# Optimization experiments

Hardware: AMD Instinct MI355X
Metric: run time of the kernel (lower is better)

The kernel has to match this reference:

```python
import jax, jax.numpy as jnp
import numpy as np

N_NODES = 100000
N_EDGES = 1600000
IN_C, HID_C, OUT_C = 64, 128, 64


def _sage_conv(x, src, dst, Wl, bl, Wr, n_nodes):
    # PyG SAGEConv (mean aggr): out = lin_l(mean_{j in N(i)} x_j) + lin_r(x_i)
    msg = x[src]  # [E, C] gather
    agg = jax.ops.segment_sum(msg, dst, num_segments=n_nodes)
    deg = jax.ops.segment_sum(jnp.ones((src.shape[0],), x.dtype), dst, num_segments=n_nodes)
    agg = agg / jnp.maximum(deg, 1.0)[:, None]
    return agg @ Wl + bl + x @ Wr


def setup_inputs() -> dict:
    key = jax.random.key(0)
    ks = jax.random.split(key, 16)
    x = jax.random.normal(ks[0], (N_NODES, IN_C), dtype=jnp.float32)
    edge_index = jax.random.randint(ks[1], (2, N_EDGES), 0, N_NODES, dtype=jnp.int64)
    s = 0.05
    return {
        "x": x,
        "edge_index": edge_index,
        # conv1: SAGEConv(IN_C, HID_C)
        "Wl1": jax.random.normal(ks[2], (IN_C, HID_C), jnp.float32) * s,
        "bl1": jnp.zeros((HID_C,), jnp.float32),
        "Wr1": jax.random.normal(ks[3], (IN_C, HID_C), jnp.float32) * s,
        # conv2: SAGEConv(HID_C, OUT_C)
        "Wl2": jax.random.normal(ks[4], (HID_C, OUT_C), jnp.float32) * s,
        "bl2": jnp.zeros((OUT_C,), jnp.float32),
        "Wr2": jax.random.normal(ks[5], (HID_C, OUT_C), jnp.float32) * s,
        # classifier MLP: OUT_C -> HID_C -> HID_C//2 -> 1
        "Wc1": jax.random.normal(ks[6], (OUT_C, HID_C), jnp.float32) * s,
        "bc1": jnp.zeros((HID_C,), jnp.float32),
        "Wc2": jax.random.normal(ks[7], (HID_C, HID_C // 2), jnp.float32) * s,
        "bc2": jnp.zeros((HID_C // 2,), jnp.float32),
        "Wc3": jax.random.normal(ks[8], (HID_C // 2, 1), jnp.float32) * s,
        "bc3": jnp.zeros((1,), jnp.float32),
    }


def reference(x, edge_index, Wl1, bl1, Wr1, Wl2, bl2, Wr2, Wc1, bc1, Wc2, bc2, Wc3, bc3):
    src, dst = edge_index[0], edge_index[1]
    n = x.shape[0]
    h = _sage_conv(x, src, dst, Wl1, bl1, Wr1, n)
    h = jax.nn.relu(h)  # dropout is identity in eval mode
    embeddings = _sage_conv(h, src, dst, Wl2, bl2, Wr2, n)
    # classifier head
    c = jax.nn.relu(embeddings @ Wc1 + bc1)
    c = jax.nn.relu(c @ Wc2 + bc2)
    fraud_probs = jax.nn.sigmoid(c @ Wc3 + bc3)
    return embeddings, fraud_probs
```

## Files before the change

### kernel.cpp

```cpp
#include <hip/hip_runtime.h>
#include <math.h>

#define N_NODES 100000
#define ZERO_NODE 100000
#define N_EDGES 1600000
#define NBKT    391
#define BCAP    5120
#define EPB     4096
#define NBLKA   391
#define PADBKT  768
#define BUCKET_CAP (N_EDGES + NBKT * PADBKT + BCAP)

using short8  = __attribute__((ext_vector_type(8))) short;
using float4v = __attribute__((ext_vector_type(4))) float;

__device__ inline unsigned short f2bf(float f) {
    unsigned int u = __float_as_uint(f);
    u += 0x7fffu + ((u >> 16) & 1u);
    return (unsigned short)(u >> 16);
}
__device__ inline float bflo(unsigned int v) { return __uint_as_float(v << 16); }
__device__ inline float bfhi(unsigned int v) { return __uint_as_float(v & 0xffff0000u); }

__global__ void prep_all(const float* __restrict__ x, unsigned short* __restrict__ xb,
                         const float* __restrict__ Wl1, const float* __restrict__ Wr1,
                         const float* __restrict__ Wl2, const float* __restrict__ Wr2,
                         const float* __restrict__ Wc1, const float* __restrict__ Wc2,
                         unsigned short* __restrict__ w1, unsigned short* __restrict__ w2,
                         unsigned short* __restrict__ wcls1, unsigned short* __restrict__ wcls2,
                         unsigned short* __restrict__ t2b) {
    int bid = blockIdx.x;
    int t = threadIdx.x;
    if (bid < 6250) {
        int i = bid * 256 + t;
        float4 v = *(const float4*)(x + (long)i * 4);
        uint2 o;
        o.x = (unsigned)f2bf(v.x) | ((unsigned)f2bf(v.y) << 16);
        o.y = (unsigned)f2bf(v.z) | ((unsigned)f2bf(v.w) << 16);
        *(uint2*)(xb + (long)i * 4) = o;
    } else if (bid < 6442) {
        int i = (bid - 6250) * 256 + t;
        if (i < 16384) {
            int n = i >> 7, k = i & 127;
            float v = (k < 64) ? Wl1[k * 128 + n] : Wr1[(k - 64) * 128 + n];
            w1[i] = f2bf(v);
        } else if (i < 32768) {
            int j = i - 16384; int n = j >> 7, k = j & 127;
            float v = (n < 64) ? Wl2[k * 64 + n] : Wr2[k * 64 + (n - 64)];
            w2[j] = f2bf(v);
        } else if (i < 40960) {
            int j = i - 32768; int n = j >> 6, k = j & 63;
            wcls1[j] = f2bf(Wc1[k * 128 + n]);
        } else {
            int j = i - 40960; int n = j >> 7, k = j & 127;
            wcls2[j] = f2bf(Wc2[k * 64 + n]);
        }
    } else {
        if (t < 32)       ((unsigned*)(xb  + (long)ZERO_NODE * 64))[t]      = 0u;
        else if (t < 64)  ((unsigned*)(t2b + (long)ZERO_NODE * 64))[t - 32] = 0u;
    }
}

__global__ __launch_bounds__(256) void binA(const int* __restrict__ esrc,
                                            const int* __restrict__ edst,
                                            int* __restrict__ bcnt,
                                            unsigned* __restrict__ stage) {
    __shared__ int hist[NBKT];
    __shared__ int rbase[NBKT];
    int t = threadIdx.x;
    for (int i = t; i < NBKT; i += 256) hist[i] = 0;
    __syncthreads();
    int e0 = blockIdx.x * EPB;
    int e1 = e0 + EPB; if (e1 > N_EDGES) e1 = N_EDGES;
    unsigned pk[16];
    int bn[16];
#pragma unroll
    for (int j = 0; j < 16; j++) {
        int e = e0 + j * 256 + t;
        bn[j] = -1;
        if (e < N_EDGES && e < e1) {
            int d = edst[e];
            int s = esrc[e];
            int b = d >> 8;
            pk[j] = (unsigned)s | ((unsigned)(d & 255) << 24);
            bn[j] = b;
            atomicAdd(&hist[b], 1);
        }
    }
    __syncthreads();
    for (int i = t; i < NBKT; i += 256) {
        int c = hist[i];
        rbase[i] = c ? atomicAdd(&bcnt[i], c) : 0;
        hist[i] = 0;
    }
    __syncthreads();
#pragma unroll
    for (int j = 0; j < 16; j++) {
        if (bn[j] >= 0) {
            int b = bn[j];
            int slot = rbase[b] + atomicAdd(&hist[b], 1);
            if (slot < BCAP)
                stage[(long)b * BCAP + slot] = pk[j];
        }
    }
}

__global__ __launch_bounds__(256) void binB(const int* __restrict__ bcnt,
                                            const unsigned* __restrict__ stage,
                                            int* __restrict__ offp, int* __restrict__ deg,
                                            int* __restrict__ bucket) {
    __shared__ int sg[512];
    __shared__ int hist[256];
    __shared__ int scn[256];
    __shared__ int lbase[256];
    int b = blockIdx.x, t = threadIdx.x;
    sg[t]       = (t < NBKT) ? bcnt[t] : 0;
    sg[t + 256] = (t + 256 < NBKT) ? bcnt[t + 256] : 0;
    hist[t] = 0;
    __syncthreads();
    for (int st = 1; st < 512; st <<= 1) {
        int a0 = (t >= st) ? sg[t - st] : 0;
        int a1 = (t + 256 >= st) ? sg[t + 256 - st] : 0;
        __syncthreads();
        sg[t] += a0; sg[t + 256] += a1;
        __syncthreads();
    }
    int cntraw = bcnt[b];
    int base = (sg[b] - cntraw) + b * PADBKT;
    int cnt = cntraw > BCAP ? BCAP : cntraw;
    const unsigned* sp = stage + (long)b * BCAP;
    unsigned pk[20];
    int nv = 0;
#pragma unroll
    for (int j = 0; j < 20; j++) {
        int i = j * 256 + t;
        if (i < cnt) {
            pk[j] = sp[i];
            atomicAdd(&hist[pk[j] >> 24], 1);
            nv = j + 1;
        }
    }
    __syncthreads();
    int v = hist[t];
    int p4 = (v + 3) & ~3;
    scn[t] = p4;
    __syncthreads();
    for (int st = 1; st < 256; st <<= 1) {
        int a = (t >= st) ? scn[t - st] : 0;
        __syncthreads();
        scn[t] += a;
        __syncthreads();
    }
    lbase[t] = scn[t] - p4;
    int node = b * 256 + t;
    if (node < N_NODES) {
        offp[node] = base + lbase[t];
        deg[node]  = v;
    }
    hist[t] = 0;
    __syncthreads();
#pragma unroll
    for (int j = 0; j < 20; j++) {
        if (j < nv) {
            unsigned p = pk[j];
            int ln = p >> 24;
            int slot = atomicAdd(&hist[ln], 1);
            bucket[base + lbase[ln] + slot] = (int)(p & 0xFFFFFFu);
        }
    }
    int ps = base + lbase[t] + v;
    int pe = base + lbase[t] + p4;
    for (int j = ps; j < pe; j++) bucket[j] = ZERO_NODE;
}

__global__ __launch_bounds__(256, 8) void gather_b(
        const unsigned short* __restrict__ y, const int* __restrict__ offp,
        const int* __restrict__ deg, const int* __restrict__ bucket,
        unsigned short* __restrict__ outb) {
    int t = threadIdx.x;
    int wv = t >> 6, lane = t & 63;
    int nh = lane >> 5;
    int g  = (lane >> 3) & 3;
    int c8 = lane & 7;
    int node = blockIdx.x * 8 + wv * 2 + nh;
    int e0 = offp[node];
    int dg = deg[node];
    int len = (dg + 3) & ~3;
    int maxlen = max(len, __shfl_xor(len, 32));
    const char* yb = (const char*)y;
    float a[8] = {0.f, 0.f, 0.f, 0.f, 0.f, 0.f, 0.f, 0.f};
    for (int base = 0; base < maxlen; base += 16) {
        uint4 v[4];
#pragma unroll
        for (int h = 0; h < 4; h++) {
            int rel = base + h * 4 + g;
            int s = bucket[e0 + rel];
            s = (rel < len) ? s : ZERO_NODE;
            unsigned off32 = ((unsigned)s << 7) + ((unsigned)c8 << 4);
            v[h] = *(const uint4*)(yb + off32);
        }
#pragma unroll
        for (int h = 0; h < 4; h++) {
            a[0] += bflo(v[h].x); a[1] += bfhi(v[h].x);
            a[2] += bflo(v[h].y); a[3] += bfhi(v[h].y);
            a[4] += bflo(v[h].z); a[5] += bfhi(v[h].z);
            a[6] += bflo(v[h].w); a[7] += bfhi(v[h].w);
        }
    }
#pragma unroll
    for (int j = 0; j < 8; j++) {
        a[j] += __shfl_xor(a[j], 8);
        a[j] += __shfl_xor(a[j], 16);
    }
    if (g == 0) {
        float sc = 1.f / fmaxf((float)dg, 1.f);
        uint4 o;
        o.x = (unsigned)f2bf(a[0]*sc) | ((unsigned)f2bf(a[1]*sc) << 16);
        o.y = (unsigned)f2bf(a[2]*sc) | ((unsigned)f2bf(a[3]*sc) << 16);
        o.z = (unsigned)f2bf(a[4]*sc) | ((unsigned)f2bf(a[5]*sc) << 16);
        o.w = (unsigned)f2bf(a[6]*sc) | ((unsigned)f2bf(a[7]*sc) << 16);
        *(uint4*)(outb + (long)node * 64 + c8 * 8) = o;
    }
}

__global__ __launch_bounds__(256, 8) void gather_badd(
        const unsigned short* __restrict__ y, const int* __restrict__ offp,
        const int* __restrict__ deg, const int* __restrict__ bucket,
        const unsigned short* __restrict__ ub, float* __restrict__ out) {
    int t = threadIdx.x;
    int wv = t >> 6, lane = t & 63;
    int nh = lane >> 5;
    int g  = (lane >> 3) & 3;
    int c8 = lane & 7;
    int node = blockIdx.x * 8 + wv * 2 + nh;
    int e0 = offp[node];
    int dg = deg[node];
    int len = (dg + 3) & ~3;
    int maxlen = max(len, __shfl_xor(len, 32));
    const char* yb = (const char*)y;
    float a[8] = {0.f, 0.f, 0.f, 0.f, 0.f, 0.f, 0.f, 0.f};
    for (int base = 0; base < maxlen; base += 16) {
        uint4 v[4];
#pragma unroll
        for (int h = 0; h < 4; h++) {
            int rel = base + h * 4 + g;
            int s = bucket[e0 + rel];
            s = (rel < len) ? s : ZERO_NODE;
            unsigned off32 = ((unsigned)s << 7) + ((unsigned)c8 << 4);
            v[h] = *(const uint4*)(yb + off32);
        }
#pragma unroll
        for (int h = 0; h < 4; h++) {
            a[0] += bflo(v[h].x); a[1] += bfhi(v[h].x);
            a[2] += bflo(v[h].y); a[3] += bfhi(v[h].y);
            a[4] += bflo(v[h].z); a[5] += bfhi(v[h].z);
            a[6] += bflo(v[h].w); a[7] += bfhi(v[h].w);
        }
    }
#pragma unroll
    for (int j = 0; j < 8; j++) {
        a[j] += __shfl_xor(a[j], 8);
        a[j] += __shfl_xor(a[j], 16);
    }
    if (g == 0) {
        float sc = 1.f / fmaxf((float)dg, 1.f);
        uint2 uv = *(const uint2*)(ub + (long)node * 64 + c8 * 8);
        float4 r0 = { a[0]*sc + bflo(uv.x), a[1]*sc + bfhi(uv.x),
                      a[2]*sc + bflo(uv.y), a[3]*sc + bfhi(uv.y) };
        uint2 uw = *(const uint2*)(ub + (long)node * 64 + c8 * 8 + 4);
        float4 r1 = { a[4]*sc + bflo(uw.x), a[5]*sc + bfhi(uw.x),
                      a[6]*sc + bflo(uw.y), a[7]*sc + bfhi(uw.y) };
        float4* op = (float4*)(out + (long)node * 64 + c8 * 8);
        op[0] = r0; op[1] = r1;
    }
}

__global__ __launch_bounds__(256, 4) void fused_conv(
        const unsigned short* __restrict__ xb, const unsigned short* __restrict__ aggb,
        const unsigned short* __restrict__ w1, const float* __restrict__ bl1,
        const unsigned short* __restrict__ w2, const float* __restrict__ bl2,
        unsigned short* __restrict__ t2b, unsigned short* __restrict__ ub) {
    __shared__ __align__(16) unsigned short smemA[64 * 136];
    __shared__ __align__(16) unsigned short smemH[64 * 136];
    unsigned short* sA = smemA;
    unsigned short* sH = smemH;
    unsigned short* stu = smemA;
    unsigned short* st2 = smemH;

    int t = threadIdx.x;
    int lane = t & 63;
    int wv = t >> 6;
    int q = lane >> 4, ln = lane & 15;

    long base = (long)blockIdx.x * 4096;
    long maxe = (long)N_NODES * 64 - 8;
#pragma unroll
    for (int it = 0; it < 2; it++) {
        int i = it * 256 + t;
        int m = i >> 3, k8 = (i & 7) * 8;
        long g = base + (long)m * 64 + k8;
        if (g > maxe) g = maxe;
        *(uint4*)(sA + m * 136 + k8)      = *(const uint4*)(aggb + g);
        *(uint4*)(sA + m * 136 + 64 + k8) = *(const uint4*)(xb + g);
    }
    __syncthreads();

    int n0 = wv * 32;
    float4v acc[2][4];
    {
        float b0 = bl1[n0 + ln], b1 = bl1[n0 + 16 + ln];
#pragma unroll
        for (int mi = 0; mi < 4; mi++) {
            acc[0][mi] = (float4v){b0, b0, b0, b0};
            acc[1][mi] = (float4v){b1, b1, b1, b1};
        }
    }
#pragma unroll
    for (int ks = 0; ks < 4; ks++) {
        int k0 = ks * 32 + q * 8;
        short8 bf0 = *(const short8*)(w1 + (long)(n0 + ln) * 128 + k0);
        short8 bf1 = *(const short8*)(w1 + (long)(n0 + 16 + ln) * 128 + k0);
#pragma unroll
        for (int mi = 0; mi < 4; mi++) {
            short8 af = *(const short8*)(sA + (mi * 16 + ln) * 136 + k0);
            acc[0][mi] = __builtin_amdgcn_mfma_f32_16x16x32_bf16(af, bf0, acc[0][mi], 0, 0, 0);
            acc[1][mi] = __builtin_amdgcn_mfma_f32_16x16x32_bf16(af, bf1, acc[1][mi], 0, 0, 0);
        }
    }
#pragma unroll
    for (int j = 0; j < 2; j++)
#pragma unroll
        for (int mi = 0; mi < 4; mi++) {
            int n = n0 + j * 16 + ln;
#pragma unroll
            for (int r = 0; r < 4; r++) {
                int m = mi * 16 + q * 4 + r;
                sH[m * 136 + n] = f2bf(fmaxf(acc[j][mi][r], 0.f));
            }
        }
    __syncthreads();

    float4v acc2[2][4];
    {
        float c0 = (n0 >= 64) ? bl2[n0 - 64 + ln] : 0.f;
        float c1 = (n0 >= 64) ? bl2[n0 - 48 + ln] : 0.f;
#pragma unroll
        for (int mi = 0; mi < 4; mi++) {
            acc2[0][mi] = (float4v){c0, c0, c0, c0};
            acc2[1][mi] = (float4v){c1, c1, c1, c1};
        }
    }
#pragma unroll
    for (int ks = 0; ks < 4; ks++) {
        int k0 = ks * 32 + q * 8;
        short8 bf0 = *(const short8*)(w2 + (long)(n0 + ln) * 128 + k0);
        short8 bf1 = *(const short8*)(w2 + (long)(n0 + 16 + ln) * 128 + k0);
#pragma unroll
        for (int mi = 0; mi < 4; mi++) {
            short8 af = *(const short8*)(sH + (mi * 16 + ln) * 136 + k0);
            acc2[0][mi] = __builtin_amdgcn_mfma_f32_16x16x32_bf16(af, bf0, acc2[0][mi], 0, 0, 0);
            acc2[1][mi] = __builtin_amdgcn_mfma_f32_16x16x32_bf16(af, bf1, acc2[1][mi], 0, 0, 0);
        }
    }
    __syncthreads();

#pragma unroll
    for (int j = 0; j < 2; j++)
#pragma unroll
        for (int mi = 0; mi < 4; mi++) {
            int n = n0 + j * 16 + ln;
#pragma unroll
            for (int r = 0; r < 4; r++) {
                int m = mi * 16 + q * 4 + r;
                if (wv < 2) st2[m * 72 + n] = f2bf(acc2[j][mi][r]);
                else        stu[m * 72 + (n - 64)] = f2bf(acc2[j][mi][r]);
            }
        }
    __syncthreads();

    long lim2 = (long)N_NODES * 32;
    unsigned* t2u = (unsigned*)t2b;
    unsigned* uu  = (unsigned*)ub;
    long ubase = base >> 1;
#pragma unroll
    for (int it = 0; it < 8; it++) {
        int i = it * 256 + t;
        long gq = ubase + i;
        if (gq < lim2) {
            int m = (i * 2) >> 6, n = (i * 2) & 63;
            t2u[gq] = (unsigned)st2[m * 72 + n] | ((unsigned)st2[m * 72 + n + 1] << 16);
            uu[gq]  = (unsigned)stu[m * 72 + n] | ((unsigned)stu[m * 72 + n + 1] << 16);
        }
    }
}

__global__ __launch_bounds__(256, 4) void fused_cls(
        const float* __restrict__ emb,
        const unsigned short* __restrict__ wcls1, const float* __restrict__ bc1,
        const unsigned short* __restrict__ wcls2, const float* __restrict__ bc2,
        const float* __restrict__ wc3, const float* __restrict__ bc3,
        float* __restrict__ probs) {
    __shared__ __align__(16) unsigned short smem[64 * 136];
    __shared__ float psum[4][64];
    unsigned short* sE = smem;
    unsigned short* sC = smem;

    int t = threadIdx.x;
    int wv = t >> 6;
    int lane = t & 63;
    int q = lane >> 4, ln = lane & 15;

    long base = (long)blockIdx.x * 4096;
    long maxe = (long)N_NODES * 64 - 4;
#pragma unroll
    for (int it = 0; it < 4; it++) {
        int i = it * 256 + t;
        int m = i >> 4, k4 = (i & 15) * 4;
        long g = base + (long)m * 64 + k4;
        if (g > maxe) g = maxe;
        float4 v = *(const float4*)(emb + g);
        uint2 o;
        o.x = (unsigned)f2bf(v.x) | ((unsigned)f2bf(v.y) << 16);
        o.y = (unsigned)f2bf(v.z) | ((unsigned)f2bf(v.w) << 16);
        *(uint2*)(sE + m * 72 + k4) = o;
    }
    __syncthreads();

    int n0 = wv * 32;
    float4v acc[2][4];
    {
        float b0 = bc1[n0 + ln], b1 = bc1[n0 + 16 + ln];
#pragma unroll
        for (int mi = 0; mi < 4; mi++) {
            acc[0][mi] = (float4v){b0, b0, b0, b0};
            acc[1][mi] = (float4v){b1, b1, b1, b1};
        }
    }
#pragma unroll
    for (int ks = 0; ks < 2; ks++) {
        int k0 = ks * 32 + q * 8;
        short8 bf0 = *(const short8*)(wcls1 + (long)(n0 + ln) * 64 + k0);
        short8 bf1 = *(const short8*)(wcls1 + (long)(n0 + 16 + ln) * 64 + k0);
#pragma unroll
        for (int mi = 0; mi < 4; mi++) {
            short8 af = *(const short8*)(sE + (mi * 16 + ln) * 72 + k0);
            acc[0][mi] = __builtin_amdgcn_mfma_f32_16x16x32_bf16(af, bf0, acc[0][mi], 0, 0, 0);
            acc[1][mi] = __builtin_amdgcn_mfma_f32_16x16x32_bf16(af, bf1, acc[1][mi], 0, 0, 0);
        }
    }
    __syncthreads();
#pragma unroll
    for (int j = 0; j < 2; j++)
#pragma unroll
        for (int mi = 0; mi < 4; mi++) {
            int n = n0 + j * 16 + ln;
#pragma unroll
            for (int r = 0; r < 4; r++) {
                int m = mi * 16 + q * 4 + r;
                sC[m * 136 + n] = f2bf(fmaxf(acc[j][mi][r], 0.f));
            }
        }
    __syncthreads();

    int n0c = wv * 16;
    float4v acc3[4];
    {
        float b = bc2[n0c + ln];
#pragma unroll
        for (int mi = 0; mi < 4; mi++) acc3[mi] = (float4v){b, b, b, b};
    }
#pragma unroll
    for (int ks = 0; ks < 4; ks++) {
        int k0 = ks * 32 + q * 8;
        short8 bf0 = *(const short8*)(wcls2 + (long)(n0c + ln) * 128 + k0);
#pragma unroll
        for (int mi = 0; mi < 4; mi++) {
            short8 af = *(const short8*)(sC + (mi * 16 + ln) * 136 + k0);
            acc3[mi] = __builtin_amdgcn_mfma_f32_16x16x32_bf16(af, bf0, acc3[mi], 0, 0, 0);
        }
    }
    float w3 = wc3[n0c + ln];
#pragma unroll
    for (int mi = 0; mi < 4; mi++)
#pragma unroll
        for (int r = 0; r < 4; r++) {
            float v = fmaxf(acc3[mi][r], 0.f) * w3;
            v += __shfl_xor(v, 1);
            v += __shfl_xor(v, 2);
            v += __shfl_xor(v, 4);
            v += __shfl_xor(v, 8);
            if (ln == 0) psum[wv][mi * 16 + q * 4 + r] = v;
        }
    __syncthreads();
    if (t < 64) {
        int node = blockIdx.x * 64 + t;
        if (node < N_NODES) {
            float tot = psum[0][t] + psum[1][t] + psum[2][t] + psum[3][t] + bc3[0];
            probs[node] = 1.f / (1.f + expf(-tot));
        }
    }
}

extern "C" void kernel_launch(void* const* d_in, const int* in_sizes, int n_in,
                              void* d_out, int out_size, void* d_ws, size_t ws_size,
                              hipStream_t stream) {
    const float* x   = (const float*)d_in[0];
    const int*   ei  = (const int*)d_in[1];
    const float* Wl1 = (const float*)d_in[2];
    const float* bl1 = (const float*)d_in[3];
    const float* Wr1 = (const float*)d_in[4];
    const float* Wl2 = (const float*)d_in[5];
    const float* bl2 = (const float*)d_in[6];
    const float* Wr2 = (const float*)d_in[7];
    const float* Wc1 = (const float*)d_in[8];
    const float* bc1 = (const float*)d_in[9];
    const float* Wc2 = (const float*)d_in[10];
    const float* bc2 = (const float*)d_in[11];
    const float* Wc3 = (const float*)d_in[12];
    const float* bc3 = (const float*)d_in[13];

    float* out = (float*)d_out;

    int* iw     = (int*)d_ws;
    int* bcnt   = iw;
    int* offp   = iw + 1024;
    int* deg    = iw + 1024 + 100352;
    int* bucket = iw + 1024 + 2 * 100352;
    unsigned* stage = (unsigned*)(bucket + BUCKET_CAP);
    size_t ioff = ((size_t)(1024 + 2 * 100352 + BUCKET_CAP) + (size_t)NBKT * BCAP) * 4;
    ioff = (ioff + 127) & ~(size_t)127;

    char* wsb = (char*)d_ws;
    unsigned short* xb    = (unsigned short*)(wsb + ioff);
    unsigned short* agg1b = xb + 6400064L;
    unsigned short* t2b   = agg1b + 6400000L;
    unsigned short* ub    = t2b + 6400064L;
    unsigned short* w1    = ub + 6400000L;
    unsigned short* w2    = w1 + 16384;
    unsigned short* wcls1 = w2 + 16384;
    unsigned short* wcls2 = wcls1 + 8192;

    float* emb   = out;
    float* probs = out + 6400000L;

    const int* esrc = ei;
    const int* edst = ei + N_EDGES;

    hipMemsetAsync(bcnt, 0, 1024 * sizeof(int), stream);

    prep_all<<<6443, 256, 0, stream>>>(x, xb, Wl1, Wr1, Wl2, Wr2, Wc1, Wc2,
                                       w1, w2, wcls1, wcls2, t2b);

    binA<<<NBLKA, 256, 0, stream>>>(esrc, edst, bcnt, stage);
    binB<<<NBKT, 256, 0, stream>>>(bcnt, stage, offp, deg, bucket);

    gather_b<<<12500, 256, 0, stream>>>(xb, offp, deg, bucket, agg1b);
    fused_conv<<<1563, 256, 0, stream>>>(xb, agg1b, w1, bl1, w2, bl2, t2b, ub);
    gather_badd<<<12500, 256, 0, stream>>>(t2b, offp, deg, bucket, ub, emb);
    fused_cls<<<1563, 256, 0, stream>>>(emb, wcls1, bc1, wcls2, bc2, Wc3, bc3, probs);
}
```

Before: 245.7 us.

## Gather neighbor features in fp8 instead of bf16 for both SAGE aggregations

Adds fp8 (e4m3) copies of x and of the layer-2 projected features, and makes both gather kernels read 64-byte fp8 rows instead of 128-byte bf16 rows. Each lane now covers 16 channels and each wave processes 8 edges per step, so node segments are padded to multiples of 8 and the bucket padding grows to match. The intent is to halve the random-gather memory traffic that dominates the aggregation kernels. The cost is extra quantization error from fp8 on the aggregated messages, which could exceed the accuracy tolerance.

```diff
diff --git a/kernel.cpp b/kernel.cpp
--- a/kernel.cpp
+++ b/kernel.cpp
@@ -8,11 +8,12 @@
 #define BCAP    5120
 #define EPB     4096
 #define NBLKA   391
-#define PADBKT  768
-#define BUCKET_CAP (N_EDGES + NBKT * PADBKT + BCAP)
+#define PADBKT  1792
+#define BUCKET_CAP (N_EDGES + NBKT * PADBKT + 2 * BCAP)
 
 using short8  = __attribute__((ext_vector_type(8))) short;
 using float4v = __attribute__((ext_vector_type(4))) float;
+using floatx2 = __attribute__((ext_vector_type(2))) float;
 
 __device__ inline unsigned short f2bf(float f) {
     unsigned int u = __float_as_uint(f);
@@ -21,14 +22,22 @@
 }
 __device__ inline float bflo(unsigned int v) { return __uint_as_float(v << 16); }
 __device__ inline float bfhi(unsigned int v) { return __uint_as_float(v & 0xffff0000u); }
+__device__ inline unsigned char f2fp8(float f) {
+    return (unsigned char)(__builtin_amdgcn_cvt_pk_fp8_f32(f, f, 0, false) & 0xff);
+}
+__device__ inline unsigned pk4fp8(float a, float b, float c, float d) {
+    unsigned p = __builtin_amdgcn_cvt_pk_fp8_f32(a, b, 0, false);
+    return __builtin_amdgcn_cvt_pk_fp8_f32(c, d, p, true);
+}
 
 __global__ void prep_all(const float* __restrict__ x, unsigned short* __restrict__ xb,
+                         unsigned* __restrict__ xq,
                          const float* __restrict__ Wl1, const float* __restrict__ Wr1,
                          const float* __restrict__ Wl2, const float* __restrict__ Wr2,
                          const float* __restrict__ Wc1, const float* __restrict__ Wc2,
                          unsigned short* __restrict__ w1, unsigned short* __restrict__ w2,
                          unsigned short* __restrict__ wcls1, unsigned short* __restrict__ wcls2,
-                         unsigned short* __restrict__ t2b) {
+                         unsigned* __restrict__ t2q) {
     int bid = blockIdx.x;
     int t = threadIdx.x;
     if (bid < 6250) {
@@ -38,6 +47,7 @@
         o.x = (unsigned)f2bf(v.x) | ((unsigned)f2bf(v.y) << 16);
         o.y = (unsigned)f2bf(v.z) | ((unsigned)f2bf(v.w) << 16);
         *(uint2*)(xb + (long)i * 4) = o;
+        xq[i] = pk4fp8(v.x, v.y, v.z, v.w);
     } else if (bid < 6442) {
         int i = (bid - 6250) * 256 + t;
         if (i < 16384) {
@@ -56,8 +66,9 @@
             wcls2[j] = f2bf(Wc2[k * 64 + n]);
         }
     } else {
-        if (t < 32)       ((unsigned*)(xb  + (long)ZERO_NODE * 64))[t]      = 0u;
-        else if (t < 64)  ((unsigned*)(t2b + (long)ZERO_NODE * 64))[t - 32] = 0u;
+        if (t < 32)       ((unsigned*)(xb + (long)ZERO_NODE * 64))[t] = 0u;
+        else if (t < 48)  xq[(long)ZERO_NODE * 16 + (t - 32)] = 0u;
+        else if (t < 64)  t2q[(long)ZERO_NODE * 16 + (t - 48)] = 0u;
     }
 }
 
@@ -142,8 +153,8 @@
     }
     __syncthreads();
     int v = hist[t];
-    int p4 = (v + 3) & ~3;
-    scn[t] = p4;
+    int p8 = (v + 7) & ~7;
+    scn[t] = p8;
     __syncthreads();
     for (int st = 1; st < 256; st <<= 1) {
         int a = (t >= st) ? scn[t - st] : 0;
@@ -151,7 +162,7 @@
         scn[t] += a;
         __syncthreads();
     }
-    lbase[t] = scn[t] - p4;
+    lbase[t] = scn[t] - p8;
     int node = b * 256 + t;
     if (node < N_NODES) {
         offp[node] = base + lbase[t];
@@ -169,109 +180,136 @@
         }
     }
     int ps = base + lbase[t] + v;
-    int pe = base + lbase[t] + p4;
+    int pe = base + lbase[t] + p8;
     for (int j = ps; j < pe; j++) bucket[j] = ZERO_NODE;
 }
 
 __global__ __launch_bounds__(256, 8) void gather_b(
-        const unsigned short* __restrict__ y, const int* __restrict__ offp,
+        const unsigned char* __restrict__ yq, const int* __restrict__ offp,
         const int* __restrict__ deg, const int* __restrict__ bucket,
         unsigned short* __restrict__ outb) {
     int t = threadIdx.x;
     int wv = t >> 6, lane = t & 63;
     int nh = lane >> 5;
-    int g  = (lane >> 3) & 3;
-    int c8 = lane & 7;
+    int g  = (lane >> 2) & 7;
+    int c16 = lane & 3;
     int node = blockIdx.x * 8 + wv * 2 + nh;
     int e0 = offp[node];
     int dg = deg[node];
-    int len = (dg + 3) & ~3;
-    int maxlen = max(len, __shfl_xor(len, 32));
-    const char* yb = (const char*)y;
-    float a[8] = {0.f, 0.f, 0.f, 0.f, 0.f, 0.f, 0.f, 0.f};
-    for (int base = 0; base < maxlen; base += 16) {
+    int len = (dg + 7) & ~7;
+    int other = __shfl_xor(len, 32);
+    int maxlen = len > other ? len : other;
+    float a[16];
+#pragma unroll
+    for (int j = 0; j < 16; j++) a[j] = 0.f;
+    for (int base = 0; base < maxlen; base += 32) {
         uint4 v[4];
 #pragma unroll
         for (int h = 0; h < 4; h++) {
-            int rel = base + h * 4 + g;
+            int rel = base + h * 8 + g;
             int s = bucket[e0 + rel];
             s = (rel < len) ? s : ZERO_NODE;
-            unsigned off32 = ((unsigned)s << 7) + ((unsigned)c8 << 4);
-            v[h] = *(const uint4*)(yb + off32);
+            unsigned off = ((unsigned)s << 6) + ((unsigned)c16 << 4);
+            v[h] = *(const uint4*)(yq + off);
         }
 #pragma unroll
         for (int h = 0; h < 4; h++) {
-            a[0] += bflo(v[h].x); a[1] += bfhi(v[h].x);
-            a[2] += bflo(v[h].y); a[3] += bfhi(v[h].y);
-            a[4] += bflo(v[h].z); a[5] += bfhi(v[h].z);
-            a[6] += bflo(v[h].w); a[7] += bfhi(v[h].w);
-        }
-    }
-#pragma unroll
-    for (int j = 0; j < 8; j++) {
+            floatx2 d;
+            d = __builtin_amdgcn_cvt_pk_f32_fp8(v[h].x, false); a[0] += d.x;  a[1] += d.y;
+            d = __builtin_amdgcn_cvt_pk_f32_fp8(v[h].x, true);  a[2] += d.x;  a[3] += d.y;
+            d = __builtin_amdgcn_cvt_pk_f32_fp8(v[h].y, false); a[4] += d.x;  a[5] += d.y;
+            d = __builtin_amdgcn_cvt_pk_f32_fp8(v[h].y, true);  a[6] += d.x;  a[7] += d.y;
+            d = __builtin_amdgcn_cvt_pk_f32_fp8(v[h].z, false); a[8] += d.x;  a[9] += d.y;
+            d = __builtin_amdgcn_cvt_pk_f32_fp8(v[h].z, true);  a[10] += d.x; a[11] += d.y;
+            d = __builtin_amdgcn_cvt_pk_f32_fp8(v[h].w, false); a[12] += d.x; a[13] += d.y;
+            d = __builtin_amdgcn_cvt_pk_f32_fp8(v[h].w, true);  a[14] += d.x; a[15] += d.y;
+        }
+    }
+#pragma unroll
+    for (int j = 0; j < 16; j++) {
+        a[j] += __shfl_xor(a[j], 4);
         a[j] += __shfl_xor(a[j], 8);
         a[j] += __shfl_xor(a[j], 16);
     }
     if (g == 0) {
         float sc = 1.f / fmaxf((float)dg, 1.f);
-        uint4 o;
-        o.x = (unsigned)f2bf(a[0]*sc) | ((unsigned)f2bf(a[1]*sc) << 16);
-        o.y = (unsigned)f2bf(a[2]*sc) | ((unsigned)f2bf(a[3]*sc) << 16);
-        o.z = (unsigned)f2bf(a[4]*sc) | ((unsigned)f2bf(a[5]*sc) << 16);
-        o.w = (unsigned)f2bf(a[6]*sc) | ((unsigned)f2bf(a[7]*sc) << 16);
-        *(uint4*)(outb + (long)node * 64 + c8 * 8) = o;
+        uint4 o0, o1;
+        o0.x = (unsigned)f2bf(a[0]*sc)  | ((unsigned)f2bf(a[1]*sc) << 16);
+        o0.y = (unsigned)f2bf(a[2]*sc)  | ((unsigned)f2bf(a[3]*sc) << 16);
+        o0.z = (unsigned)f2bf(a[4]*sc)  | ((unsigned)f2bf(a[5]*sc) << 16);
+        o0.w = (unsigned)f2bf(a[6]*sc)  | ((unsigned)f2bf(a[7]*sc) << 16);
+        o1.x = (unsigned)f2bf(a[8]*sc)  | ((unsigned)f2bf(a[9]*sc) << 16);
+        o1.y = (unsigned)f2bf(a[10]*sc) | ((unsigned)f2bf(a[11]*sc) << 16);
+        o1.z = (unsigned)f2bf(a[12]*sc) | ((unsigned)f2bf(a[13]*sc) << 16);
+        o1.w = (unsigned)f2bf(a[14]*sc) | ((unsigned)f2bf(a[15]*sc) << 16);
+        unsigned short* op = outb + (long)node * 64 + c16 * 16;
+        *(uint4*)op = o0;
+        *(uint4*)(op + 8) = o1;
     }
 }
 
 __global__ __launch_bounds__(256, 8) void gather_badd(
-        const unsigned short* __restrict__ y, const int* __restrict__ offp,
+        const unsigned char* __restrict__ yq, const int* __restrict__ offp,
         const int* __restrict__ deg, const int* __restrict__ bucket,
         const unsigned short* __restrict__ ub, float* __restrict__ out) {
     int t = threadIdx.x;
     int wv = t >> 6, lane = t & 63;
     int nh = lane >> 5;
-    int g  = (lane >> 3) & 3;
-    int c8 = lane & 7;
+    int g  = (lane >> 2) & 7;
+    int c16 = lane & 3;
     int node = blockIdx.x * 8 + wv * 2 + nh;
     int e0 = offp[node];
     int dg = deg[node];
-    int len = (dg + 3) & ~3;
-    int maxlen = max(len, __shfl_xor(len, 32));
-    const char* yb = (const char*)y;
-    float a[8] = {0.f, 0.f, 0.f, 0.f, 0.f, 0.f, 0.f, 0.f};
-    for (int base = 0; base < maxlen; base += 16) {
+    int len = (dg + 7) & ~7;
+    int other = __shfl_xor(len, 32);
+    int maxlen = len > other ? len : other;
+    float a[16];
+#pragma unroll
+    for (int j = 0; j < 16; j++) a[j] = 0.f;
+    for (int base = 0; base < maxlen; base += 32) {
         uint4 v[4];
 #pragma unroll
         for (int h = 0; h < 4; h++) {
-            int rel = base + h * 4 + g;
+            int rel = base + h * 8 + g;
             int s = bucket[e0 + rel];
             s = (rel < len) ? s : ZERO_NODE;
-            unsigned off32 = ((unsigned)s << 7) + ((unsigned)c8 << 4);
-            v[h] = *(const uint4*)(yb + off32);
+            unsigned off = ((unsigned)s << 6) + ((unsigned)c16 << 4);
+            v[h] = *(const uint4*)(yq + off);
         }
 #pragma unroll
         for (int h = 0; h < 4; h++) {
-            a[0] += bflo(v[h].x); a[1] += bfhi(v[h].x);
-            a[2] += bflo(v[h].y); a[3] += bfhi(v[h].y);
-            a[4] += bflo(v[h].z); a[5] += bfhi(v[h].z);
-            a[6] += bflo(v[h].w); a[7] += bfhi(v[h].w);
-        }
-    }
-#pragma unroll
-    for (int j = 0; j < 8; j++) {
+            floatx2 d;
+            d = __builtin_amdgcn_cvt_pk_f32_fp8(v[h].x, false); a[0] += d.x;  a[1] += d.y;
+            d = __builtin_amdgcn_cvt_pk_f32_fp8(v[h].x, true);  a[2] += d.x;  a[3] += d.y;
+            d = __builtin_amdgcn_cvt_pk_f32_fp8(v[h].y, false); a[4] += d.x;  a[5] += d.y;
+            d = __builtin_amdgcn_cvt_pk_f32_fp8(v[h].y, true);  a[6] += d.x;  a[7] += d.y;
+            d = __builtin_amdgcn_cvt_pk_f32_fp8(v[h].z, false); a[8] += d.x;  a[9] += d.y;
+            d = __builtin_amdgcn_cvt_pk_f32_fp8(v[h].z, true);  a[10] += d.x; a[11] += d.y;
+            d = __builtin_amdgcn_cvt_pk_f32_fp8(v[h].w, false); a[12] += d.x; a[13] += d.y;
+            d = __builtin_amdgcn_cvt_pk_f32_fp8(v[h].w, true);  a[14] += d.x; a[15] += d.y;
+        }
+    }
+#pragma unroll
+    for (int j = 0; j < 16; j++) {
+        a[j] += __shfl_xor(a[j], 4);
         a[j] += __shfl_xor(a[j], 8);
         a[j] += __shfl_xor(a[j], 16);
     }
     if (g == 0) {
         float sc = 1.f / fmaxf((float)dg, 1.f);
-        uint2 uv = *(const uint2*)(ub + (long)node * 64 + c8 * 8);
-        float4 r0 = { a[0]*sc + bflo(uv.x), a[1]*sc + bfhi(uv.x),
-                      a[2]*sc + bflo(uv.y), a[3]*sc + bfhi(uv.y) };
-        uint2 uw = *(const uint2*)(ub + (long)node * 64 + c8 * 8 + 4);
-        float4 r1 = { a[4]*sc + bflo(uw.x), a[5]*sc + bfhi(uw.x),
-                      a[6]*sc + bflo(uw.y), a[7]*sc + bfhi(uw.y) };
-        float4* op = (float4*)(out + (long)node * 64 + c8 * 8);
-        op[0] = r0; op[1] = r1;
+        const unsigned short* up = ub + (long)node * 64 + c16 * 16;
+        uint4 u0 = *(const uint4*)up;
+        uint4 u1 = *(const uint4*)(up + 8);
+        float4 r0 = { a[0]*sc + bflo(u0.x), a[1]*sc + bfhi(u0.x),
+                      a[2]*sc + bflo(u0.y), a[3]*sc + bfhi(u0.y) };
+        float4 r1 = { a[4]*sc + bflo(u0.z), a[5]*sc + bfhi(u0.z),
+                      a[6]*sc + bflo(u0.w), a[7]*sc + bfhi(u0.w) };
+        float4 r2 = { a[8]*sc + bflo(u1.x), a[9]*sc + bfhi(u1.x),
+                      a[10]*sc + bflo(u1.y), a[11]*sc + bfhi(u1.y) };
+        float4 r3 = { a[12]*sc + bflo(u1.z), a[13]*sc + bfhi(u1.z),
+                      a[14]*sc + bflo(u1.w), a[15]*sc + bfhi(u1.w) };
+        float4* op = (float4*)(out + (long)node * 64 + c16 * 16);
+        op[0] = r0; op[1] = r1; op[2] = r2; op[3] = r3;
     }
 }
 
@@ -279,13 +317,13 @@
         const unsigned short* __restrict__ xb, const unsigned short* __restrict__ aggb,
         const unsigned short* __restrict__ w1, const float* __restrict__ bl1,
         const unsigned short* __restrict__ w2, const float* __restrict__ bl2,
-        unsigned short* __restrict__ t2b, unsigned short* __restrict__ ub) {
+        unsigned* __restrict__ t2q, unsigned short* __restrict__ ub) {
     __shared__ __align__(16) unsigned short smemA[64 * 136];
     __shared__ __align__(16) unsigned short smemH[64 * 136];
     unsigned short* sA = smemA;
     unsigned short* sH = smemH;
     unsigned short* stu = smemA;
-    unsigned short* st2 = smemH;
+    unsigned char*  st2q = (unsigned char*)smemH;
 
     int t = threadIdx.x;
     int lane = t & 63;
@@ -372,15 +410,25 @@
 #pragma unroll
             for (int r = 0; r < 4; r++) {
                 int m = mi * 16 + q * 4 + r;
-                if (wv < 2) st2[m * 72 + n] = f2bf(acc2[j][mi][r]);
+                if (wv < 2) st2q[m * 80 + n] = f2fp8(acc2[j][mi][r]);
                 else        stu[m * 72 + (n - 64)] = f2bf(acc2[j][mi][r]);
             }
         }
     __syncthreads();
 
+    long qbase = (long)blockIdx.x * 1024;
+    long qlim = (long)N_NODES * 16;
+#pragma unroll
+    for (int it = 0; it < 4; it++) {
+        int i = it * 256 + t;
+        long gq = qbase + i;
+        if (gq < qlim) {
+            int m = i >> 4, dw = i & 15;
+            t2q[gq] = *(const unsigned*)(st2q + m * 80 + dw * 4);
+        }
+    }
     long lim2 = (long)N_NODES * 32;
-    unsigned* t2u = (unsigned*)t2b;
-    unsigned* uu  = (unsigned*)ub;
+    unsigned* uu = (unsigned*)ub;
     long ubase = base >> 1;
 #pragma unroll
     for (int it = 0; it < 8; it++) {
@@ -388,8 +436,7 @@
         long gq = ubase + i;
         if (gq < lim2) {
             int m = (i * 2) >> 6, n = (i * 2) & 63;
-            t2u[gq] = (unsigned)st2[m * 72 + n] | ((unsigned)st2[m * 72 + n + 1] << 16);
-            uu[gq]  = (unsigned)stu[m * 72 + n] | ((unsigned)stu[m * 72 + n + 1] << 16);
+            uu[gq] = (unsigned)stu[m * 72 + n] | ((unsigned)stu[m * 72 + n + 1] << 16);
         }
     }
 }
@@ -533,9 +580,10 @@
     char* wsb = (char*)d_ws;
     unsigned short* xb    = (unsigned short*)(wsb + ioff);
     unsigned short* agg1b = xb + 6400064L;
-    unsigned short* t2b   = agg1b + 6400000L;
-    unsigned short* ub    = t2b + 6400064L;
-    unsigned short* w1    = ub + 6400000L;
+    unsigned short* ub    = agg1b + 6400000L;
+    unsigned*       xq    = (unsigned*)(ub + 6400000L);
+    unsigned*       t2q   = xq + 1600016L;
+    unsigned short* w1    = (unsigned short*)(t2q + 1600016L);
     unsigned short* w2    = w1 + 16384;
     unsigned short* wcls1 = w2 + 16384;
     unsigned short* wcls2 = wcls1 + 8192;
@@ -548,14 +596,14 @@
 
     hipMemsetAsync(bcnt, 0, 1024 * sizeof(int), stream);
 
-    prep_all<<<6443, 256, 0, stream>>>(x, xb, Wl1, Wr1, Wl2, Wr2, Wc1, Wc2,
-                                       w1, w2, wcls1, wcls2, t2b);
+    prep_all<<<6443, 256, 0, stream>>>(x, xb, xq, Wl1, Wr1, Wl2, Wr2, Wc1, Wc2,
+                                       w1, w2, wcls1, wcls2, t2q);
 
     binA<<<NBLKA, 256, 0, stream>>>(esrc, edst, bcnt, stage);
     binB<<<NBKT, 256, 0, stream>>>(bcnt, stage, offp, deg, bucket);
 
-    gather_b<<<12500, 256, 0, stream>>>(xb, offp, deg, bucket, agg1b);
-    fused_conv<<<1563, 256, 0, stream>>>(xb, agg1b, w1, bl1, w2, bl2, t2b, ub);
-    gather_badd<<<12500, 256, 0, stream>>>(t2b, offp, deg, bucket, ub, emb);
+    gather_b<<<12500, 256, 0, stream>>>((const unsigned char*)xq, offp, deg, bucket, agg1b);
+    fused_conv<<<1563, 256, 0, stream>>>(xb, agg1b, w1, bl1, w2, bl2, t2q, ub);
+    gather_badd<<<12500, 256, 0, stream>>>((const unsigned char*)t2q, offp, deg, bucket, ub, emb);
     fused_cls<<<1563, 256, 0, stream>>>(emb, wcls1, bc1, wcls2, bc2, Wc3, bc3, probs);
 }
```

After: 417.9 us. 70.1% more time.
